# Kernel optimization log

Hardware: AMD Instinct MI355X
Metric: run time of the kernel (lower is better)

Reference implementation:

```python
import jax, jax.numpy as jnp
import numpy as np

B, D, H, W, C = 1, 16, 56, 56, 256
WD, WH, WW = 2, 7, 7
SD, SH, SW = 1, 3, 3
HEADS = 8
HDIM = C // HEADS
N = WD * WH * WW          # 98 tokens per window
NW = (D // WD) * (H // WH) * (W // WW)  # 512 windows per batch element
HID = 4 * C


def _rel_index():
    coords = np.stack(np.meshgrid(np.arange(WD), np.arange(WH), np.arange(WW), indexing='ij')).reshape(3, -1)
    rel = (coords[:, :, None] - coords[:, None, :]).transpose(1, 2, 0).astype(np.int64)
    rel[..., 0] += WD - 1; rel[..., 1] += WH - 1; rel[..., 2] += WW - 1
    rel[..., 0] *= (2 * WH - 1) * (2 * WW - 1)
    rel[..., 1] *= (2 * WW - 1)
    return rel.sum(-1)  # (N, N)

REL_INDEX = jnp.asarray(_rel_index())


def _np_window_partition(x):
    b, d, h, w, c = x.shape
    x = x.reshape(b, d // WD, WD, h // WH, WH, w // WW, WW, c)
    return x.transpose(0, 1, 3, 5, 2, 4, 6, 7).reshape(-1, N, c)


def _compute_mask():
    # Swin compute_mask: label 3x3x3 shifted regions, windows mask cross-region pairs with -100
    img = np.zeros((1, D, H, W, 1), np.float32)
    cnt = 0
    for ds in (slice(0, -WD), slice(-WD, -SD), slice(-SD, None)):
        for hs in (slice(0, -WH), slice(-WH, -SH), slice(-SH, None)):
            for ws in (slice(0, -WW), slice(-WW, -SW), slice(-SW, None)):
                img[:, ds, hs, ws, :] = cnt; cnt += 1
    mw = _np_window_partition(img).reshape(NW, N)
    am = mw[:, None, :] - mw[:, :, None]
    return np.where(am != 0, -100.0, 0.0).astype(np.float32)


def setup_inputs():
    key = jax.random.key(0)
    ks = jax.random.split(key, 8)
    s = 0.02
    return {
        'x': jax.random.normal(ks[0], (B, D, H, W, C), jnp.float32),
        'mask_matrix': jnp.asarray(_compute_mask()),
        'g1': jnp.ones((C,), jnp.float32), 'b1': jnp.zeros((C,), jnp.float32),
        'qkv_w': jax.random.normal(ks[1], (C, 3 * C), jnp.float32) * s,
        'qkv_b': jnp.zeros((3 * C,), jnp.float32),
        'rpb': jax.random.normal(ks[2], ((2 * WD - 1) * (2 * WH - 1) * (2 * WW - 1), HEADS), jnp.float32) * s,
        'proj_w': jax.random.normal(ks[3], (C, C), jnp.float32) * s,
        'proj_b': jnp.zeros((C,), jnp.float32),
        'g2': jnp.ones((C,), jnp.float32), 'b2': jnp.zeros((C,), jnp.float32),
        'fc1_w': jax.random.normal(ks[4], (C, HID), jnp.float32) * s,
        'fc1_b': jnp.zeros((HID,), jnp.float32),
        'fc2_w': jax.random.normal(ks[5], (HID, C), jnp.float32) * s,
        'fc2_b': jnp.zeros((C,), jnp.float32),
    }


def _ln(x, g, b):
    mu = jnp.mean(x, -1, keepdims=True)
    var = jnp.mean((x - mu) ** 2, -1, keepdims=True)
    return (x - mu) * jax.lax.rsqrt(var + 1e-5) * g + b


def _window_partition(x):
    b = x.shape[0]
    x = x.reshape(b, D // WD, WD, H // WH, WH, W // WW, WW, C)
    return x.transpose(0, 1, 3, 5, 2, 4, 6, 7).reshape(-1, N, C)


def _window_reverse(w):
    x = w.reshape(B, D // WD, H // WH, W // WW, WD, WH, WW, C)
    return x.transpose(0, 1, 4, 2, 5, 3, 6, 7).reshape(B, D, H, W, C)


def reference(x, mask_matrix, g1, b1, qkv_w, qkv_b, rpb, proj_w, proj_b, g2, b2, fc1_w, fc1_b, fc2_w, fc2_b):
    shortcut = x
    y = _ln(x, g1, b1)
    # D,H,W divide window sizes -> pad amounts are 0; cyclic shift for SW-MSA
    y = jnp.roll(y, shift=(-SD, -SH, -SW), axis=(1, 2, 3))
    xw = _window_partition(y)                          # (B_, N, C)
    B_ = xw.shape[0]
    qkv = (xw @ qkv_w + qkv_b).reshape(B_, N, 3, HEADS, HDIM)
    q, k, v = jnp.moveaxis(qkv, 2, 0)                  # each (B_, N, HEADS, HDIM)
    q = q * (HDIM ** -0.5)
    attn = jnp.einsum('bnhd,bmhd->bhnm', q, k)         # (B_, HEADS, N, N)
    bias = rpb[REL_INDEX.reshape(-1)].reshape(N, N, HEADS).transpose(2, 0, 1)
    attn = attn + bias[None]
    attn = attn.reshape(B_ // NW, NW, HEADS, N, N) + mask_matrix[None, :, None]
    attn = jax.nn.softmax(attn.reshape(B_, HEADS, N, N), axis=-1)
    out = jnp.einsum('bhnm,bmhd->bnhd', attn, v).reshape(B_, N, C)
    out = out @ proj_w + proj_b
    y = _window_reverse(out)
    y = jnp.roll(y, shift=(SD, SH, SW), axis=(1, 2, 3))
    x = shortcut + y
    h = _ln(x, g2, b2)
    h = jax.nn.gelu(h @ fc1_w + fc1_b, approximate=False)
    h = h @ fc2_w + fc2_b
    return x + h
```

## Files before the change

### kernel.cpp

```cpp
#include <hip/hip_runtime.h>
#include <hip/hip_bf16.h>

typedef __hip_bfloat16 bf16;
typedef __attribute__((ext_vector_type(4))) float f32x4;
typedef __attribute__((ext_vector_type(8))) short bf16x8;

#define MFMA16(a,b,c) __builtin_amdgcn_mfma_f32_16x16x32_bf16((a),(b),(c),0,0,0)

static __device__ inline unsigned short bfbits(float f) {
  __hip_bfloat16 h = __float2bfloat16(f);
  union { __hip_bfloat16 h; unsigned short u; } u;
  u.h = h; return u.u;
}
static __device__ inline float bf2f(unsigned short u) {
  return __uint_as_float(((unsigned int)u) << 16);
}
static __device__ inline void gld16(const void* g, void* l) {
  __builtin_amdgcn_global_load_lds((const __attribute__((address_space(1))) void*)g,
                                   (__attribute__((address_space(3))) void*)l, 16, 0, 0);
}

__global__ __launch_bounds__(256) void transpose_w(const float* __restrict__ src,
                                                   bf16* __restrict__ dst,
                                                   int N, int K, int scaleN, float scale) {
  int idx = blockIdx.x * 256 + threadIdx.x;
  if (idx >= N * K) return;
  int n = idx / K, k = idx - n * K;
  float v = src[(size_t)k * N + n];
  if (n < scaleN) v *= scale;
  dst[idx] = __float2bfloat16(v);
}

__global__ __launch_bounds__(256) void bias_table_bf(const float* __restrict__ rpb,
                                                     unsigned short* __restrict__ biasT) {
  int idx = blockIdx.x * 256 + threadIdx.x;
  if (idx >= 98 * 98) return;
  int nn = idx / 98, mm = idx - nn * 98;
  int ld = nn / 49, lrem = nn - ld * 49, lh = lrem / 7, lw = lrem - lh * 7;
  int md = mm / 49, mrem = mm - md * 49, mh = mrem / 7, mw = mrem - mh * 7;
  int rel = (ld - md + 1) * 169 + (lh - mh + 6) * 13 + (lw - mw + 6);
  #pragma unroll
  for (int h = 0; h < 8; ++h)
    biasT[h * 9604 + mm * 98 + nn] = bfbits(rpb[rel * 8 + h]);
}

__global__ __launch_bounds__(256) void vtrans_k(const unsigned short* __restrict__ v,
                                                unsigned short* __restrict__ vt) {
  __shared__ unsigned short S[98 * 33];
  const unsigned short* src = v + (size_t)blockIdx.x * 3136;
  for (int i = threadIdx.x; i < 3136; i += 256) {
    int n = i >> 5, d = i & 31;
    S[n * 33 + d] = src[i];
  }
  __syncthreads();
  unsigned short* dst = vt + ((size_t)blockIdx.x << 12);
  for (int i = threadIdx.x; i < 4096; i += 256) {
    int d = i >> 7, m = i & 127;
    dst[i] = (m < 98) ? S[m * 33 + d] : (unsigned short)0;
  }
}

__global__ __launch_bounds__(256) void ln_k(const float* __restrict__ x,
                                            const float* __restrict__ g,
                                            const float* __restrict__ bias,
                                            bf16* __restrict__ out, int windowed) {
  const int wid = threadIdx.x >> 6, lane = threadIdx.x & 63;
  const int t = blockIdx.x * 4 + wid;
  int src = t;
  if (windowed) {
    int widx = t / 98, n = t - widx * 98;
    int zd = widx >> 6, zh = (widx >> 3) & 7, zw = widx & 7;
    int ld = n / 49, rem = n - ld * 49, lh = rem / 7, lw = rem - lh * 7;
    int d = zd * 2 + ld, h = zh * 7 + lh, w = zw * 7 + lw;
    int dsrc = (d + 1) & 15;
    int hsrc = h + 3; if (hsrc >= 56) hsrc -= 56;
    int wsrc = w + 3; if (wsrc >= 56) wsrc -= 56;
    src = (dsrc * 56 + hsrc) * 56 + wsrc;
  }
  const float4 v = *(const float4*)(x + (size_t)src * 256 + lane * 4);
  float s1 = v.x + v.y + v.z + v.w;
  float s2 = v.x * v.x + v.y * v.y + v.z * v.z + v.w * v.w;
  #pragma unroll
  for (int d = 1; d < 64; d <<= 1) {
    s1 += __shfl_xor(s1, d);
    s2 += __shfl_xor(s2, d);
  }
  float mu = s1 * (1.f / 256.f);
  float var = s2 * (1.f / 256.f) - mu * mu;
  float rs = rsqrtf(var + 1e-5f);
  const float4 gv = *(const float4*)(g + lane * 4);
  const float4 bv = *(const float4*)(bias + lane * 4);
  ushort4 pk;
  pk.x = bfbits((v.x - mu) * rs * gv.x + bv.x);
  pk.y = bfbits((v.y - mu) * rs * gv.y + bv.y);
  pk.z = bfbits((v.z - mu) * rs * gv.z + bv.z);
  pk.w = bfbits((v.w - mu) * rs * gv.w + bv.w);
  *(ushort4*)((unsigned short*)out + (size_t)t * 256 + lane * 4) = pk;
}

template<int EPI>
__global__ __launch_bounds__(256) void gemm_k(const bf16* __restrict__ A,
                                              const bf16* __restrict__ Bt,
                                              const float* __restrict__ bias,
                                              int N, int K, int mrow0,
                                              bf16* __restrict__ out_bf,
                                              float* __restrict__ out_f,
                                              const float* __restrict__ add_f) {
  __shared__ bf16 As[128 * 32];
  __shared__ bf16 Bs[128 * 32];
  const int tid = threadIdx.x;
  const int wid = tid >> 6, lane = tid & 63;
  const int row0 = blockIdx.y * 128, col0 = blockIdx.x * 128;
  const int lrow = tid >> 2, lcol = (tid & 3) * 8;
  const int fr = lane & 15, kh = lane >> 4;
  const int wm = (wid >> 1) * 64, wn = (wid & 1) * 64;
  f32x4 zero4 = {0.f, 0.f, 0.f, 0.f};
  f32x4 acc[4][4];
  #pragma unroll
  for (int i = 0; i < 4; ++i)
    #pragma unroll
    for (int j = 0; j < 4; ++j) acc[i][j] = zero4;

  const bf16* aP = A + (size_t)(row0 + lrow) * K + lcol;
  const bf16* bP = Bt + (size_t)(col0 + lrow) * K + lcol;
  bf16* asD = &As[lrow * 32 + lcol];
  bf16* bsD = &Bs[lrow * 32 + lcol];

  for (int k0 = 0; k0 < K; k0 += 32) {
    __syncthreads();
    gld16(aP + k0, asD);
    gld16(aP + (size_t)64 * K + k0, asD + 64 * 32);
    gld16(bP + k0, bsD);
    gld16(bP + (size_t)64 * K + k0, bsD + 64 * 32);
    __syncthreads();
    bf16x8 af[4], bfr[4];
    #pragma unroll
    for (int i = 0; i < 4; ++i)
      af[i] = *(const bf16x8*)&As[(wm + i * 16 + fr) * 32 + kh * 8];
    #pragma unroll
    for (int j = 0; j < 4; ++j)
      bfr[j] = *(const bf16x8*)&Bs[(wn + j * 16 + fr) * 32 + kh * 8];
    #pragma unroll
    for (int i = 0; i < 4; ++i)
      #pragma unroll
      for (int j = 0; j < 4; ++j)
        acc[i][j] = MFMA16(af[i], bfr[j], acc[i][j]);
  }

  #pragma unroll
  for (int i = 0; i < 4; ++i) {
    #pragma unroll
    for (int j = 0; j < 4; ++j) {
      #pragma unroll
      for (int r = 0; r < 4; ++r) {
        int row = row0 + wm + i * 16 + kh * 4 + r;
        int col = col0 + wn + j * 16 + fr;
        float bb = bias[col];
        if (EPI == 0 && col < 256) bb *= 0.17677669529663687f;
        float v = acc[i][j][r] + bb;
        if (EPI == 0) {
          int part = col >> 8, head = (col >> 5) & 7, hd = col & 31;
          int widx = row / 98, n = row - widx * 98;
          size_t off = ((size_t)(part * 512 + widx) * 8 + head) * 3136 + (size_t)n * 32 + hd;
          out_bf[off] = __float2bfloat16(v);
        } else if (EPI == 1) {
          int widx = row / 98, n = row - widx * 98;
          int zd = widx >> 6, zh = (widx >> 3) & 7, zw = widx & 7;
          int ld = n / 49, rem = n - ld * 49, lh = rem / 7, lw = rem - lh * 7;
          int d = zd * 2 + ld, h = zh * 7 + lh, w = zw * 7 + lw;
          int dsrc = (d + 1) & 15;
          int hsrc = h + 3; if (hsrc >= 56) hsrc -= 56;
          int wsrc = w + 3; if (wsrc >= 56) wsrc -= 56;
          size_t tok = (size_t)(dsrc * 56 + hsrc) * 56 + wsrc;
          out_f[tok * 256 + col] = add_f[tok * 256 + col] + v;
        } else if (EPI == 2) {
          float gl = 0.5f * v * (1.0f + erff(v * 0.70710678118654752f));
          out_bf[(size_t)row * 1024 + col] = __float2bfloat16(gl);
        } else {
          size_t ro = (size_t)(mrow0 + row);
          out_f[ro * 256 + col] = add_f[ro * 256 + col] + v;
        }
      }
    }
  }
}

__global__ __launch_bounds__(256, 2) void attn_k(const bf16* __restrict__ qkv,
                                                 const unsigned short* __restrict__ vt,
                                                 const unsigned short* __restrict__ bias_bf,
                                                 bf16* __restrict__ out) {
  __shared__ unsigned short Pl[112 * 128];
  __shared__ unsigned short biasS[98 * 100];
  __shared__ unsigned char lblS[112];
  const int tid = threadIdx.x;
  const int widx = blockIdx.x >> 1, hh = blockIdx.x & 1;
  const int wid = tid >> 6, lane = tid & 63;
  const int fr = lane & 15, kh = lane >> 4, kh4 = kh * 4;
  const int tr0 = wid * 2;
  f32x4 zero4 = {0.f, 0.f, 0.f, 0.f};

  if (tid < 112) {
    unsigned char l = 255;
    if (tid < 98) {
      int zd = widx >> 6, zh = (widx >> 3) & 7, zw = widx & 7;
      int ld = tid / 49, rem = tid - ld * 49, lh = rem / 7, lw = rem - lh * 7;
      int d = zd * 2 + ld, h = zh * 7 + lh, w = zw * 7 + lw;
      int cd = (d >= 14) + (d >= 15);
      int ch = (h >= 49) + (h >= 53);
      int cw = (w >= 49) + (w >= 53);
      l = (unsigned char)(cd * 9 + ch * 3 + cw);
    }
    lblS[tid] = l;
  }
  __syncthreads();

  unsigned int lblK[7];
  #pragma unroll
  for (int mt = 0; mt < 7; ++mt)
    lblK[mt] = *(const unsigned int*)&lblS[mt * 16 + kh4];
  const bool t1v = (tr0 + 1) < 7;
  unsigned int lq0 = 0x01010101u * lblS[tr0 * 16 + fr];
  unsigned int lq1 = 0x01010101u * lblS[(t1v ? tr0 + 1 : 0) * 16 + fr];

  for (int it = 0; it < 4; ++it) {
    const int head = hh * 4 + it;
    const unsigned short* qbu = (const unsigned short*)qkv + ((size_t)widx * 8 + head) * 3136;
    const unsigned short* kbu = qbu + (size_t)12845056;
    const unsigned short* brow = bias_bf + head * 9604;
    const unsigned short* vtb = vt + (((size_t)widx * 8 + head) << 12);

    __syncthreads();
    for (int j = tid; j < 4802; j += 256) {
      int n = j / 49, m2 = (j - n * 49) * 2;
      *(unsigned int*)&biasS[n * 100 + m2] = *(const unsigned int*)(brow + n * 98 + m2);
    }

    int qr0 = tr0 * 16 + fr; if (qr0 > 97) qr0 = 97;
    int qr1 = (tr0 + 1) * 16 + fr; if (qr1 > 97) qr1 = 97;
    bf16x8 aq0 = *(const bf16x8*)(qbu + qr0 * 32 + kh * 8);
    bf16x8 aq1 = *(const bf16x8*)(qbu + qr1 * 32 + kh * 8);

    f32x4 s2[2][7];
    #pragma unroll
    for (int a = 0; a < 2; ++a)
      #pragma unroll
      for (int m = 0; m < 7; ++m) s2[a][m] = zero4;
    #pragma unroll
    for (int mt = 0; mt < 7; ++mt) {
      int krow = mt * 16 + fr; if (krow > 97) krow = 97;
      bf16x8 kf = *(const bf16x8*)(kbu + krow * 32 + kh * 8);
      s2[0][mt] = MFMA16(kf, aq0, s2[0][mt]);
      s2[1][mt] = MFMA16(kf, aq1, s2[1][mt]);
    }
    __syncthreads();

    #pragma unroll
    for (int ti = 0; ti < 2; ++ti) {
      int tr = tr0 + ti;
      if (tr < 7) {
        int q = tr * 16 + fr;
        bool rv = q < 98;
        int qc = rv ? q : 0;
        unsigned int lq = (ti == 0) ? lq0 : lq1;
        float mx = -1e30f;
        #pragma unroll
        for (int mt = 0; mt < 7; ++mt) {
          unsigned int df = lblK[mt] ^ lq;
          #pragma unroll
          for (int r = 0; r < 4; ++r) {
            int k = mt * 16 + kh4 + r;
            bool ok = rv && (k < 98);
            float b = bf2f(biasS[(k < 98 ? k : 0) * 100 + qc]);
            float msk = ((df >> (8 * r)) & 255u) ? -100.f : 0.f;
            float sv = ok ? (s2[ti][mt][r] + b + msk) : -1e30f;
            s2[ti][mt][r] = sv;
            mx = fmaxf(mx, sv);
          }
        }
        mx = fmaxf(mx, __shfl_xor(mx, 16));
        mx = fmaxf(mx, __shfl_xor(mx, 32));
        float sum = 0.f;
        #pragma unroll
        for (int mt = 0; mt < 7; ++mt) {
          #pragma unroll
          for (int r = 0; r < 4; ++r) {
            float sv = s2[ti][mt][r];
            float e = (sv > -1e29f) ? __expf(sv - mx) : 0.f;
            s2[ti][mt][r] = e;
            sum += e;
          }
        }
        sum += __shfl_xor(sum, 16);
        sum += __shfl_xor(sum, 32);
        float inv = rv ? (1.0f / sum) : 0.f;
        #pragma unroll
        for (int mt = 0; mt < 7; ++mt) {
          ushort4 pk;
          pk.x = bfbits(s2[ti][mt][0] * inv);
          pk.y = bfbits(s2[ti][mt][1] * inv);
          pk.z = bfbits(s2[ti][mt][2] * inv);
          pk.w = bfbits(s2[ti][mt][3] * inv);
          *(ushort4*)&Pl[(q * 128 + mt * 16 + kh4) ^ ((q & 7) << 3)] = pk;
        }
        ushort4 zz; zz.x = zz.y = zz.z = zz.w = 0;
        *(ushort4*)&Pl[(q * 128 + 112 + kh4) ^ ((q & 7) << 3)] = zz;
      }
    }

    f32x4 o00 = zero4, o01 = zero4, o10 = zero4, o11 = zero4;
    #pragma unroll
    for (int kk = 0; kk < 4; ++kk) {
      bf16x8 vv0 = *(const bf16x8*)(vtb + fr * 128 + kk * 32 + kh * 8);
      bf16x8 vv1 = *(const bf16x8*)(vtb + (16 + fr) * 128 + kk * 32 + kh * 8);
      int prow0 = tr0 * 16 + fr;
      bf16x8 pa0 = *(const bf16x8*)&((const bf16*)Pl)[(prow0 * 128 + kk * 32 + kh * 8) ^ ((prow0 & 7) << 3)];
      o00 = MFMA16(pa0, vv0, o00);
      o01 = MFMA16(pa0, vv1, o01);
      if (t1v) {
        int prow1 = prow0 + 16;
        bf16x8 pa1 = *(const bf16x8*)&((const bf16*)Pl)[(prow1 * 128 + kk * 32 + kh * 8) ^ ((prow1 & 7) << 3)];
        o10 = MFMA16(pa1, vv0, o10);
        o11 = MFMA16(pa1, vv1, o11);
      }
    }
    #pragma unroll
    for (int r = 0; r < 4; ++r) {
      int row = tr0 * 16 + kh4 + r;
      if (row < 98) {
        size_t grow = (size_t)widx * 98 + row;
        out[grow * 256 + head * 32 + fr] = __float2bfloat16(o00[r]);
        out[grow * 256 + head * 32 + 16 + fr] = __float2bfloat16(o01[r]);
      }
    }
    if (t1v) {
      #pragma unroll
      for (int r = 0; r < 4; ++r) {
        int row = (tr0 + 1) * 16 + kh4 + r;
        if (row < 98) {
          size_t grow = (size_t)widx * 98 + row;
          out[grow * 256 + head * 32 + fr] = __float2bfloat16(o10[r]);
          out[grow * 256 + head * 32 + 16 + fr] = __float2bfloat16(o11[r]);
        }
      }
    }
  }
}

extern "C" void kernel_launch(void* const* d_in, const int* in_sizes, int n_in,
                              void* d_out, int out_size, void* d_ws, size_t ws_size,
                              hipStream_t stream) {
  const float* x      = (const float*)d_in[0];
  const float* g1     = (const float*)d_in[2];
  const float* b1     = (const float*)d_in[3];
  const float* qkv_w  = (const float*)d_in[4];
  const float* qkv_b  = (const float*)d_in[5];
  const float* rpb    = (const float*)d_in[6];
  const float* proj_w = (const float*)d_in[7];
  const float* proj_b = (const float*)d_in[8];
  const float* g2     = (const float*)d_in[9];
  const float* b2     = (const float*)d_in[10];
  const float* fc1_w  = (const float*)d_in[11];
  const float* fc1_b  = (const float*)d_in[12];
  const float* fc2_w  = (const float*)d_in[13];
  const float* fc2_b  = (const float*)d_in[14];
  float* outp = (float*)d_out;

  char* ws = (char*)d_ws;
  if (ws_size < (size_t)156237824) return;
  bf16*  wqkvT   = (bf16*)(ws + 0);
  bf16*  wprojT  = (bf16*)(ws + 393216);
  bf16*  wfc1T   = (bf16*)(ws + 524288);
  bf16*  wfc2T   = (bf16*)(ws + 1048576);
  unsigned short* bias_bf = (unsigned short*)(ws + 1572864);
  float* x2      = (float*)(ws + 2097152);
  unsigned short* vtb = (unsigned short*)(ws + 11931648);
  char*  pool    = ws + 53477376;
  bf16*  xw       = (bf16*)pool;
  bf16*  qkvb     = (bf16*)(pool + 25690112);
  bf16*  attn_out = (bf16*)pool;
  bf16*  hbuf     = (bf16*)pool;
  bf16*  hh       = (bf16*)(pool + 25690112);

  transpose_w<<<768, 256, 0, stream>>>(qkv_w, wqkvT, 768, 256, 256, 0.17677669529663687f);
  transpose_w<<<256, 256, 0, stream>>>(proj_w, wprojT, 256, 256, 0, 1.f);
  transpose_w<<<1024, 256, 0, stream>>>(fc1_w, wfc1T, 1024, 256, 0, 1.f);
  transpose_w<<<1024, 256, 0, stream>>>(fc2_w, wfc2T, 256, 1024, 0, 1.f);
  bias_table_bf<<<38, 256, 0, stream>>>(rpb, bias_bf);

  ln_k<<<12544, 256, 0, stream>>>(x, g1, b1, xw, 1);
  gemm_k<0><<<dim3(6, 392), 256, 0, stream>>>(xw, wqkvT, qkv_b, 768, 256, 0, qkvb, nullptr, nullptr);
  vtrans_k<<<4096, 256, 0, stream>>>((const unsigned short*)qkvb + (size_t)2 * 12845056, vtb);
  attn_k<<<1024, 256, 0, stream>>>(qkvb, vtb, bias_bf, attn_out);
  gemm_k<1><<<dim3(2, 392), 256, 0, stream>>>(attn_out, wprojT, proj_b, 256, 256, 0, nullptr, x2, x);
  ln_k<<<12544, 256, 0, stream>>>(x2, g2, b2, hbuf, 0);
  for (int ch = 0; ch < 2; ++ch) {
    gemm_k<2><<<dim3(8, 196), 256, 0, stream>>>(hbuf + (size_t)ch * 25088 * 256, wfc1T, fc1_b,
                                                1024, 256, 0, hh, nullptr, nullptr);
    gemm_k<3><<<dim3(2, 196), 256, 0, stream>>>(hh, wfc2T, fc2_b, 256, 1024, ch * 25088,
                                                nullptr, outp, x2);
  }
}
```

Baseline: 356.6 us.

## Double-buffer GEMM LDS tiles and remap blocks across XCDs

The GEMM kernel now uses two LDS buffers and issues the global-to-LDS loads for the next K tile before computing on the current one, with one barrier per iteration instead of two. The grid is flattened to 1D and block indices are permuted so that consecutive tiles are spread across the 8 XCDs in contiguous chunks, which aims at better L2 reuse. LDS use doubles. The barrier placement relies on the async global_load_lds finishing before the next iteration's sync.

```diff
diff --git a/kernel.cpp b/kernel.cpp
--- a/kernel.cpp
+++ b/kernel.cpp
@@ -102,15 +102,18 @@
 __global__ __launch_bounds__(256) void gemm_k(const bf16* __restrict__ A,
                                               const bf16* __restrict__ Bt,
                                               const float* __restrict__ bias,
-                                              int N, int K, int mrow0,
+                                              int N, int K, int NX, int mrow0,
                                               bf16* __restrict__ out_bf,
                                               float* __restrict__ out_f,
                                               const float* __restrict__ add_f) {
-  __shared__ bf16 As[128 * 32];
-  __shared__ bf16 Bs[128 * 32];
+  __shared__ bf16 As[2][128 * 32];
+  __shared__ bf16 Bs[2][128 * 32];
   const int tid = threadIdx.x;
   const int wid = tid >> 6, lane = tid & 63;
-  const int row0 = blockIdx.y * 128, col0 = blockIdx.x * 128;
+  const int q8 = gridDim.x >> 3;
+  const int tile = (blockIdx.x & 7) * q8 + (blockIdx.x >> 3);
+  const int bx = tile % NX, by = tile / NX;
+  const int row0 = by * 128, col0 = bx * 128;
   const int lrow = tid >> 2, lcol = (tid & 3) * 8;
   const int fr = lane & 15, kh = lane >> 4;
   const int wm = (wid >> 1) * 64, wn = (wid & 1) * 64;
@@ -123,28 +126,42 @@
 
   const bf16* aP = A + (size_t)(row0 + lrow) * K + lcol;
   const bf16* bP = Bt + (size_t)(col0 + lrow) * K + lcol;
-  bf16* asD = &As[lrow * 32 + lcol];
-  bf16* bsD = &Bs[lrow * 32 + lcol];
-
-  for (int k0 = 0; k0 < K; k0 += 32) {
+  bf16* asD = &As[0][lrow * 32 + lcol];
+  bf16* bsD = &Bs[0][lrow * 32 + lcol];
+
+  const int nk = K >> 5;
+  gld16(aP, asD);
+  gld16(aP + (size_t)64 * K, asD + 2048);
+  gld16(bP, bsD);
+  gld16(bP + (size_t)64 * K, bsD + 2048);
+
+  int cur = 0;
+  for (int t = 0; t < nk; ++t) {
     __syncthreads();
-    gld16(aP + k0, asD);
-    gld16(aP + (size_t)64 * K + k0, asD + 64 * 32);
-    gld16(bP + k0, bsD);
-    gld16(bP + (size_t)64 * K + k0, bsD + 64 * 32);
-    __syncthreads();
+    if (t + 1 < nk) {
+      int k0 = (t + 1) * 32;
+      bf16* aD = asD + (cur ^ 1) * 4096;
+      bf16* bD = bsD + (cur ^ 1) * 4096;
+      gld16(aP + k0, aD);
+      gld16(aP + (size_t)64 * K + k0, aD + 2048);
+      gld16(bP + k0, bD);
+      gld16(bP + (size_t)64 * K + k0, bD + 2048);
+    }
+    const bf16* Ab = As[cur];
+    const bf16* Bb = Bs[cur];
     bf16x8 af[4], bfr[4];
     #pragma unroll
     for (int i = 0; i < 4; ++i)
-      af[i] = *(const bf16x8*)&As[(wm + i * 16 + fr) * 32 + kh * 8];
+      af[i] = *(const bf16x8*)&Ab[(wm + i * 16 + fr) * 32 + kh * 8];
     #pragma unroll
     for (int j = 0; j < 4; ++j)
-      bfr[j] = *(const bf16x8*)&Bs[(wn + j * 16 + fr) * 32 + kh * 8];
+      bfr[j] = *(const bf16x8*)&Bb[(wn + j * 16 + fr) * 32 + kh * 8];
     #pragma unroll
     for (int i = 0; i < 4; ++i)
       #pragma unroll
       for (int j = 0; j < 4; ++j)
         acc[i][j] = MFMA16(af[i], bfr[j], acc[i][j]);
+    cur ^= 1;
   }
 
   #pragma unroll
@@ -388,15 +405,15 @@
   bias_table_bf<<<38, 256, 0, stream>>>(rpb, bias_bf);
 
   ln_k<<<12544, 256, 0, stream>>>(x, g1, b1, xw, 1);
-  gemm_k<0><<<dim3(6, 392), 256, 0, stream>>>(xw, wqkvT, qkv_b, 768, 256, 0, qkvb, nullptr, nullptr);
+  gemm_k<0><<<2352, 256, 0, stream>>>(xw, wqkvT, qkv_b, 768, 256, 6, 0, qkvb, nullptr, nullptr);
   vtrans_k<<<4096, 256, 0, stream>>>((const unsigned short*)qkvb + (size_t)2 * 12845056, vtb);
   attn_k<<<1024, 256, 0, stream>>>(qkvb, vtb, bias_bf, attn_out);
-  gemm_k<1><<<dim3(2, 392), 256, 0, stream>>>(attn_out, wprojT, proj_b, 256, 256, 0, nullptr, x2, x);
+  gemm_k<1><<<784, 256, 0, stream>>>(attn_out, wprojT, proj_b, 256, 256, 2, 0, nullptr, x2, x);
   ln_k<<<12544, 256, 0, stream>>>(x2, g2, b2, hbuf, 0);
   for (int ch = 0; ch < 2; ++ch) {
-    gemm_k<2><<<dim3(8, 196), 256, 0, stream>>>(hbuf + (size_t)ch * 25088 * 256, wfc1T, fc1_b,
-                                                1024, 256, 0, hh, nullptr, nullptr);
-    gemm_k<3><<<dim3(2, 196), 256, 0, stream>>>(hh, wfc2T, fc2_b, 256, 1024, ch * 25088,
-                                                nullptr, outp, x2);
-  }
-}
+    gemm_k<2><<<1568, 256, 0, stream>>>(hbuf + (size_t)ch * 25088 * 256, wfc1T, fc1_b,
+                                        1024, 256, 8, 0, hh, nullptr, nullptr);
+    gemm_k<3><<<392, 256, 0, stream>>>(hh, wfc2T, fc2_b, 256, 1024, 2, ch * 25088,
+                                       nullptr, outp, x2);
+  }
+}
```

Measured after the change: 326.9 us. 8.3% less time.
